# Optimization experiments

Measured on AMD Instinct MI355X. Metric: run time of the kernel, lower is better.

Reference implementation:

```python
import jax, jax.numpy as jnp
import numpy as np
from jax import lax

VOCAB, EMBED, HIDDEN, SEQ = 50257, 1024, 1024, 4096


def setup_inputs() -> dict:
    key = jax.random.key(0)
    ks = jax.random.split(key, 8)
    s = 0.02
    return {
        "input_seq": jax.random.randint(ks[0], (SEQ,), 0, VOCAB),
        "emb": jax.random.normal(ks[1], (VOCAB, EMBED), jnp.float32) * s,
        "Wrx": jax.random.normal(ks[2], (HIDDEN, EMBED), jnp.float32) * s,
        "Wrh": jax.random.normal(ks[3], (HIDDEN, HIDDEN), jnp.float32) * s,
        "Wzx": jax.random.normal(ks[4], (HIDDEN, EMBED), jnp.float32) * s,
        "Wzh": jax.random.normal(ks[5], (HIDDEN, HIDDEN), jnp.float32) * s,
        "Wx": jax.random.normal(ks[6], (HIDDEN, EMBED), jnp.float32) * s,
        "Wh": jax.random.normal(ks[7], (HIDDEN, HIDDEN), jnp.float32) * s,
    }


def reference(input_seq, emb, Wrx, Wrh, Wzx, Wzh, Wx, Wh):
    # Embed whole sequence at once: [S, E]
    x_seq = emb[input_seq]
    # Hoist input-side projections out of the recurrence (one GEMM each): [S, H]
    xr = x_seq @ Wrx.T
    xz = x_seq @ Wzx.T
    xh = x_seq @ Wx.T

    def step(h, xs):
        xr_t, xz_t, xh_t = xs
        z = jax.nn.sigmoid(xz_t + Wzh @ h)          # update gate
        r = jax.nn.sigmoid(xr_t + Wrh @ h)          # reset gate
        h_tilde = jnp.tanh(xh_t + Wh @ (r * h))     # candidate
        h_new = z * h + (1.0 - z) * h_tilde
        return h_new, None

    h0 = jnp.zeros((Wh.shape[0],), dtype=emb.dtype)
    h_final, _ = lax.scan(step, h0, (xr, xz, xh))
    return h_final
```

## Files before the change

kernel.cpp:

```cpp
#include <hip/hip_runtime.h>
#include <stdint.h>


#define HID    1024
#define SEQLEN 4096
#define NWG    128
#define RPW    8
#define BLOCK  256

typedef unsigned long long u64;

__global__ __launch_bounds__(BLOCK) void proj_gemm(
    const int* __restrict__ seq, const float* __restrict__ emb,
    const float* __restrict__ Wrx, const float* __restrict__ Wzx,
    const float* __restrict__ Wx,
    float* __restrict__ xr, float* __restrict__ xz, float* __restrict__ xh)
{
  __shared__ float As[32][68];
  __shared__ float Bs[32][68];
  __shared__ int   idx[64];

  const float* W = (blockIdx.z == 0) ? Wrx : (blockIdx.z == 1) ? Wzx : Wx;
  float*       C = (blockIdx.z == 0) ? xr  : (blockIdx.z == 1) ? xz  : xh;

  const int tid = threadIdx.x;
  const int t0 = blockIdx.y * 64;
  const int i0 = blockIdx.x * 64;
  if (tid < 64) idx[tid] = seq[t0 + tid];
  __syncthreads();

  float acc[4][4] = {};
  const int tx = tid & 15, ty = tid >> 4;
  const int c4 = (tid & 7) * 4;
  const int r8 = tid >> 3;

  for (int k0 = 0; k0 < HID; k0 += 32) {
    for (int l = 0; l < 2; ++l) {
      const int rr = r8 + l * 32;
      float4 av = *(const float4*)(emb + (size_t)idx[rr] * HID + k0 + c4);
      As[c4+0][rr]=av.x; As[c4+1][rr]=av.y; As[c4+2][rr]=av.z; As[c4+3][rr]=av.w;
      float4 bv = *(const float4*)(W + (size_t)(i0 + rr) * HID + k0 + c4);
      Bs[c4+0][rr]=bv.x; Bs[c4+1][rr]=bv.y; Bs[c4+2][rr]=bv.z; Bs[c4+3][rr]=bv.w;
    }
    __syncthreads();
    #pragma unroll
    for (int k = 0; k < 32; ++k) {
      float a[4], b[4];
      *(float4*)a = *(const float4*)&As[k][ty * 4];
      *(float4*)b = *(const float4*)&Bs[k][tx * 4];
      #pragma unroll
      for (int i = 0; i < 4; ++i)
        #pragma unroll
        for (int j = 0; j < 4; ++j)
          acc[i][j] = fmaf(a[i], b[j], acc[i][j]);
    }
    __syncthreads();
  }
  #pragma unroll
  for (int i = 0; i < 4; ++i) {
    float4 v = make_float4(acc[i][0], acc[i][1], acc[i][2], acc[i][3]);
    *(float4*)(C + (size_t)(t0 + ty * 4 + i) * HID + i0 + tx * 4) = v;
  }
}

__device__ __forceinline__ u64 pack_cell(float v, unsigned tag) {
  return ((u64)tag << 32) | (u64)__float_as_uint(v);
}

__device__ __forceinline__ void poll4(const u64* __restrict__ cells, int j0,
                                      unsigned want, float v[4], int* budget) {
  u64 c0 = 0, c1 = 0, c2 = 0, c3 = 0;
  bool d0 = false, d1 = false, d2 = false, d3 = false;
  for (;;) {
    if (!d0) { c0 = __hip_atomic_load(&cells[j0+0], __ATOMIC_RELAXED, __HIP_MEMORY_SCOPE_AGENT); d0 = (unsigned)(c0 >> 32) == want; }
    if (!d1) { c1 = __hip_atomic_load(&cells[j0+1], __ATOMIC_RELAXED, __HIP_MEMORY_SCOPE_AGENT); d1 = (unsigned)(c1 >> 32) == want; }
    if (!d2) { c2 = __hip_atomic_load(&cells[j0+2], __ATOMIC_RELAXED, __HIP_MEMORY_SCOPE_AGENT); d2 = (unsigned)(c2 >> 32) == want; }
    if (!d3) { c3 = __hip_atomic_load(&cells[j0+3], __ATOMIC_RELAXED, __HIP_MEMORY_SCOPE_AGENT); d3 = (unsigned)(c3 >> 32) == want; }
    if (d0 & d1 & d2 & d3) break;
    if (--(*budget) <= 0) break;
  }
  v[0] = __uint_as_float((unsigned)c0);
  v[1] = __uint_as_float((unsigned)c1);
  v[2] = __uint_as_float((unsigned)c2);
  v[3] = __uint_as_float((unsigned)c3);
}

__global__ __launch_bounds__(BLOCK) void rnn_scan(
    const float* __restrict__ Wzh, const float* __restrict__ Wrh,
    const float* __restrict__ Whh,
    const float* __restrict__ xz, const float* __restrict__ xr,
    const float* __restrict__ xh,
    u64* __restrict__ hcell,
    u64* __restrict__ rhcell,
    float* __restrict__ out)
{
  const int tid  = threadIdx.x;
  const int wave = tid >> 6, lane = tid & 63;
  const int g    = blockIdx.x;
  const int r0   = g * RPW;
  const int rowA = r0 + wave * 2;
  const int j0   = tid * 4;

  __shared__ float h_lds[HID];
  __shared__ float rh_lds[HID];

  float wgt[3][2][16];
  #pragma unroll
  for (int m = 0; m < 3; ++m) {
    const float* Wm = (m == 0) ? Wzh : (m == 1) ? Wrh : Whh;
    #pragma unroll
    for (int rr = 0; rr < 2; ++rr) {
      const float* p = Wm + (size_t)(rowA + rr) * HID + lane * 16;
      #pragma unroll
      for (int c = 0; c < 16; c += 4) {
        float4 v = *(const float4*)(p + c);
        wgt[m][rr][c+0] = v.x; wgt[m][rr][c+1] = v.y;
        wgt[m][rr][c+2] = v.z; wgt[m][rr][c+3] = v.w;
      }
    }
  }

  int budget = 1 << 22;
  float xzv[2], xrv[2], xhv[2], zv[2];

  for (int t = 1; t <= SEQLEN; ++t) {
    const u64* hsrc = hcell + ((t - 1) & 1) * HID;
    u64* rdst = rhcell + (t & 1) * HID;

    if (lane == 0) {
      #pragma unroll
      for (int rr = 0; rr < 2; ++rr) {
        xzv[rr] = xz[(size_t)(t - 1) * HID + rowA + rr];
        xrv[rr] = xr[(size_t)(t - 1) * HID + rowA + rr];
        xhv[rr] = xh[(size_t)(t - 1) * HID + rowA + rr];
      }
    }

    float hv[4];
    poll4(hsrc, j0, (unsigned)(t - 1), hv, &budget);
    *(float4*)&h_lds[j0] = make_float4(hv[0], hv[1], hv[2], hv[3]);
    __syncthreads();

    float hr[16];
    #pragma unroll
    for (int c = 0; c < 16; c += 4)
      *(float4*)&hr[c] = *(const float4*)&h_lds[lane * 16 + c];
    float az[2] = {0.f, 0.f}, ar[2] = {0.f, 0.f};
    #pragma unroll
    for (int rr = 0; rr < 2; ++rr)
      #pragma unroll
      for (int c = 0; c < 16; ++c) {
        az[rr] = fmaf(wgt[0][rr][c], hr[c], az[rr]);
        ar[rr] = fmaf(wgt[1][rr][c], hr[c], ar[rr]);
      }
    #pragma unroll
    for (int m = 1; m < 64; m <<= 1) {
      az[0] += __shfl_xor(az[0], m, 64);
      az[1] += __shfl_xor(az[1], m, 64);
      ar[0] += __shfl_xor(ar[0], m, 64);
      ar[1] += __shfl_xor(ar[1], m, 64);
    }
    if (lane == 0) {
      #pragma unroll
      for (int rr = 0; rr < 2; ++rr) {
        zv[rr]    = 1.f / (1.f + __expf(-(xzv[rr] + az[rr])));
        float rg  = 1.f / (1.f + __expf(-(xrv[rr] + ar[rr])));
        float rh  = rg * h_lds[rowA + rr];
        __hip_atomic_store(&rdst[rowA + rr], pack_cell(rh, (unsigned)t),
                           __ATOMIC_RELAXED, __HIP_MEMORY_SCOPE_AGENT);
      }
    }

    float rv[4];
    poll4(rdst, j0, (unsigned)t, rv, &budget);
    *(float4*)&rh_lds[j0] = make_float4(rv[0], rv[1], rv[2], rv[3]);
    __syncthreads();

    float rr16[16];
    #pragma unroll
    for (int c = 0; c < 16; c += 4)
      *(float4*)&rr16[c] = *(const float4*)&rh_lds[lane * 16 + c];
    float ac[2] = {0.f, 0.f};
    #pragma unroll
    for (int rr = 0; rr < 2; ++rr)
      #pragma unroll
      for (int c = 0; c < 16; ++c)
        ac[rr] = fmaf(wgt[2][rr][c], rr16[c], ac[rr]);
    #pragma unroll
    for (int m = 1; m < 64; m <<= 1) {
      ac[0] += __shfl_xor(ac[0], m, 64);
      ac[1] += __shfl_xor(ac[1], m, 64);
    }
    if (lane == 0) {
      #pragma unroll
      for (int rr = 0; rr < 2; ++rr) {
        float cand  = tanhf(xhv[rr] + ac[rr]);
        float hprev = h_lds[rowA + rr];
        float hn    = zv[rr] * hprev + (1.f - zv[rr]) * cand;
        __hip_atomic_store(&hcell[(t & 1) * HID + rowA + rr],
                           pack_cell(hn, (unsigned)t),
                           __ATOMIC_RELAXED, __HIP_MEMORY_SCOPE_AGENT);
        if (t == SEQLEN) out[rowA + rr] = hn;
      }
    }
    __syncthreads();
  }
}

extern "C" void kernel_launch(void* const* d_in, const int* in_sizes, int n_in,
                              void* d_out, int out_size, void* d_ws, size_t ws_size,
                              hipStream_t stream) {
  (void)in_sizes; (void)n_in; (void)out_size; (void)ws_size;

  const int*   seq = (const int*)d_in[0];
  const float* emb = (const float*)d_in[1];
  const float* Wrx = (const float*)d_in[2];
  const float* Wrh = (const float*)d_in[3];
  const float* Wzx = (const float*)d_in[4];
  const float* Wzh = (const float*)d_in[5];
  const float* Wx  = (const float*)d_in[6];
  const float* Wh  = (const float*)d_in[7];

  char* ws = (char*)d_ws;
  const size_t PROJ = (size_t)SEQLEN * HID * sizeof(float);
  float* xr = (float*)(ws);
  float* xz = (float*)(ws + PROJ);
  float* xh = (float*)(ws + 2 * PROJ);
  u64* hcell  = (u64*)(ws + 3 * PROJ);
  u64* rhcell = (u64*)(ws + 3 * PROJ + 2 * HID * sizeof(u64));

  hipMemsetAsync(hcell, 0xFF, 4 * HID * sizeof(u64), stream);
  hipMemsetAsync(hcell, 0x00, HID * sizeof(u64), stream);

  proj_gemm<<<dim3(HID / 64, SEQLEN / 64, 3), BLOCK, 0, stream>>>(
      seq, emb, Wrx, Wzx, Wx, xr, xz, xh);

  rnn_scan<<<dim3(NWG), BLOCK, 0, stream>>>(
      Wzh, Wrh, Wh, xz, xr, xh, hcell, rhcell, (float*)d_out);
}
```

Baseline: 26.33 ms.

## Replace tagged per-element cells with per-workgroup flags and coherent float buffers

Drops the 64-bit tagged value cells. Each workgroup now writes plain floats to double-buffered h and r*h arrays, then publishes one release flag per step. Consumers poll a single flag per pair of threads with s_sleep backoff and read the data with a cache-bypassing float4 load. This is meant to cut the number of polled atomic loads and halve the bytes moved per exchange, at the cost of an extra __syncthreads and a release-flag hop per phase. It also moves the weight and LDS indexing to a strided layout so LDS reads are bank-friendly.

```diff
diff --git a/kernel.cpp b/kernel.cpp
--- a/kernel.cpp
+++ b/kernel.cpp
@@ -63,35 +63,36 @@
   }
 }
 
-__device__ __forceinline__ u64 pack_cell(float v, unsigned tag) {
-  return ((u64)tag << 32) | (u64)__float_as_uint(v);
-}
-
-__device__ __forceinline__ void poll4(const u64* __restrict__ cells, int j0,
-                                      unsigned want, float v[4], int* budget) {
-  u64 c0 = 0, c1 = 0, c2 = 0, c3 = 0;
-  bool d0 = false, d1 = false, d2 = false, d3 = false;
+__device__ __forceinline__ float4 load_f4_coherent(const float* p) {
+  float4 v;
+  asm volatile("global_load_dwordx4 %0, %1, off sc0 sc1\n\ts_waitcnt vmcnt(0)"
+               : "=v"(v) : "v"(p) : "memory");
+  return v;
+}
+__device__ __forceinline__ void store_f2_coherent(float* p, float a, float b) {
+  u64 v = ((u64)__float_as_uint(b) << 32) | (u64)__float_as_uint(a);
+  __hip_atomic_store((u64*)p, v, __ATOMIC_RELAXED, __HIP_MEMORY_SCOPE_AGENT);
+}
+
+__device__ __forceinline__ void poll_flag(const u64* f, u64 want, int* budget) {
   for (;;) {
-    if (!d0) { c0 = __hip_atomic_load(&cells[j0+0], __ATOMIC_RELAXED, __HIP_MEMORY_SCOPE_AGENT); d0 = (unsigned)(c0 >> 32) == want; }
-    if (!d1) { c1 = __hip_atomic_load(&cells[j0+1], __ATOMIC_RELAXED, __HIP_MEMORY_SCOPE_AGENT); d1 = (unsigned)(c1 >> 32) == want; }
-    if (!d2) { c2 = __hip_atomic_load(&cells[j0+2], __ATOMIC_RELAXED, __HIP_MEMORY_SCOPE_AGENT); d2 = (unsigned)(c2 >> 32) == want; }
-    if (!d3) { c3 = __hip_atomic_load(&cells[j0+3], __ATOMIC_RELAXED, __HIP_MEMORY_SCOPE_AGENT); d3 = (unsigned)(c3 >> 32) == want; }
-    if (d0 & d1 & d2 & d3) break;
+    u64 v = __hip_atomic_load((u64*)f, __ATOMIC_RELAXED, __HIP_MEMORY_SCOPE_AGENT);
+    if (v >= want) break;
+    __builtin_amdgcn_s_sleep(1);
     if (--(*budget) <= 0) break;
   }
-  v[0] = __uint_as_float((unsigned)c0);
-  v[1] = __uint_as_float((unsigned)c1);
-  v[2] = __uint_as_float((unsigned)c2);
-  v[3] = __uint_as_float((unsigned)c3);
-}
-
-__global__ __launch_bounds__(BLOCK) void rnn_scan(
+  asm volatile("" ::: "memory");
+}
+
+__global__ __launch_bounds__(BLOCK, 1) void rnn_scan(
     const float* __restrict__ Wzh, const float* __restrict__ Wrh,
     const float* __restrict__ Whh,
     const float* __restrict__ xz, const float* __restrict__ xr,
     const float* __restrict__ xh,
-    u64* __restrict__ hcell,
-    u64* __restrict__ rhcell,
+    float* __restrict__ hbuf,
+    float* __restrict__ rhbuf,
+    u64* __restrict__ fh,
+    u64* __restrict__ frh,
     float* __restrict__ out)
 {
   const int tid  = threadIdx.x;
@@ -100,6 +101,7 @@
   const int r0   = g * RPW;
   const int rowA = r0 + wave * 2;
   const int j0   = tid * 4;
+  const int src  = tid >> 1;
 
   __shared__ float h_lds[HID];
   __shared__ float rh_lds[HID];
@@ -110,23 +112,20 @@
     const float* Wm = (m == 0) ? Wzh : (m == 1) ? Wrh : Whh;
     #pragma unroll
     for (int rr = 0; rr < 2; ++rr) {
-      const float* p = Wm + (size_t)(rowA + rr) * HID + lane * 16;
-      #pragma unroll
-      for (int c = 0; c < 16; c += 4) {
-        float4 v = *(const float4*)(p + c);
-        wgt[m][rr][c+0] = v.x; wgt[m][rr][c+1] = v.y;
-        wgt[m][rr][c+2] = v.z; wgt[m][rr][c+3] = v.w;
+      const float* p = Wm + (size_t)(rowA + rr) * HID + lane * 4;
+      #pragma unroll
+      for (int q = 0; q < 4; ++q) {
+        float4 v = *(const float4*)(p + q * 256);
+        wgt[m][rr][q*4+0] = v.x; wgt[m][rr][q*4+1] = v.y;
+        wgt[m][rr][q*4+2] = v.z; wgt[m][rr][q*4+3] = v.w;
       }
     }
   }
 
   int budget = 1 << 22;
-  float xzv[2], xrv[2], xhv[2], zv[2];
+  float xzv[2], xrv[2], xhv[2], zv[2], hprev[2];
 
   for (int t = 1; t <= SEQLEN; ++t) {
-    const u64* hsrc = hcell + ((t - 1) & 1) * HID;
-    u64* rdst = rhcell + (t & 1) * HID;
-
     if (lane == 0) {
       #pragma unroll
       for (int rr = 0; rr < 2; ++rr) {
@@ -136,15 +135,19 @@
       }
     }
 
-    float hv[4];
-    poll4(hsrc, j0, (unsigned)(t - 1), hv, &budget);
-    *(float4*)&h_lds[j0] = make_float4(hv[0], hv[1], hv[2], hv[3]);
+    if (t == 1) {
+      *(float4*)&h_lds[j0] = make_float4(0.f, 0.f, 0.f, 0.f);
+    } else {
+      poll_flag(&fh[src], (u64)(t - 1), &budget);
+      float4 hv = load_f4_coherent(hbuf + ((t - 1) & 1) * HID + j0);
+      *(float4*)&h_lds[j0] = hv;
+    }
     __syncthreads();
 
     float hr[16];
     #pragma unroll
-    for (int c = 0; c < 16; c += 4)
-      *(float4*)&hr[c] = *(const float4*)&h_lds[lane * 16 + c];
+    for (int q = 0; q < 4; ++q)
+      *(float4*)&hr[q*4] = *(const float4*)&h_lds[q * 256 + lane * 4];
     float az[2] = {0.f, 0.f}, ar[2] = {0.f, 0.f};
     #pragma unroll
     for (int rr = 0; rr < 2; ++rr)
@@ -161,25 +164,31 @@
       ar[1] += __shfl_xor(ar[1], m, 64);
     }
     if (lane == 0) {
+      float rh[2];
       #pragma unroll
       for (int rr = 0; rr < 2; ++rr) {
+        hprev[rr] = h_lds[rowA + rr];
         zv[rr]    = 1.f / (1.f + __expf(-(xzv[rr] + az[rr])));
         float rg  = 1.f / (1.f + __expf(-(xrv[rr] + ar[rr])));
-        float rh  = rg * h_lds[rowA + rr];
-        __hip_atomic_store(&rdst[rowA + rr], pack_cell(rh, (unsigned)t),
-                           __ATOMIC_RELAXED, __HIP_MEMORY_SCOPE_AGENT);
-      }
-    }
-
-    float rv[4];
-    poll4(rdst, j0, (unsigned)t, rv, &budget);
-    *(float4*)&rh_lds[j0] = make_float4(rv[0], rv[1], rv[2], rv[3]);
+        rh[rr]    = rg * hprev[rr];
+      }
+      store_f2_coherent(rhbuf + (t & 1) * HID + rowA, rh[0], rh[1]);
+    }
+    __syncthreads();
+    if (tid == 0)
+      __hip_atomic_store(&frh[g], (u64)t, __ATOMIC_RELEASE, __HIP_MEMORY_SCOPE_AGENT);
+
+    poll_flag(&frh[src], (u64)t, &budget);
+    {
+      float4 rv = load_f4_coherent(rhbuf + (t & 1) * HID + j0);
+      *(float4*)&rh_lds[j0] = rv;
+    }
     __syncthreads();
 
     float rr16[16];
     #pragma unroll
-    for (int c = 0; c < 16; c += 4)
-      *(float4*)&rr16[c] = *(const float4*)&rh_lds[lane * 16 + c];
+    for (int q = 0; q < 4; ++q)
+      *(float4*)&rr16[q*4] = *(const float4*)&rh_lds[q * 256 + lane * 4];
     float ac[2] = {0.f, 0.f};
     #pragma unroll
     for (int rr = 0; rr < 2; ++rr)
@@ -192,18 +201,18 @@
       ac[1] += __shfl_xor(ac[1], m, 64);
     }
     if (lane == 0) {
+      float hn[2];
       #pragma unroll
       for (int rr = 0; rr < 2; ++rr) {
-        float cand  = tanhf(xhv[rr] + ac[rr]);
-        float hprev = h_lds[rowA + rr];
-        float hn    = zv[rr] * hprev + (1.f - zv[rr]) * cand;
-        __hip_atomic_store(&hcell[(t & 1) * HID + rowA + rr],
-                           pack_cell(hn, (unsigned)t),
-                           __ATOMIC_RELAXED, __HIP_MEMORY_SCOPE_AGENT);
-        if (t == SEQLEN) out[rowA + rr] = hn;
-      }
-    }
-    __syncthreads();
+        float cand = tanhf(xhv[rr] + ac[rr]);
+        hn[rr]     = zv[rr] * hprev[rr] + (1.f - zv[rr]) * cand;
+      }
+      store_f2_coherent(hbuf + (t & 1) * HID + rowA, hn[0], hn[1]);
+      if (t == SEQLEN) { out[rowA] = hn[0]; out[rowA + 1] = hn[1]; }
+    }
+    __syncthreads();
+    if (tid == 0)
+      __hip_atomic_store(&fh[g], (u64)t, __ATOMIC_RELEASE, __HIP_MEMORY_SCOPE_AGENT);
   }
 }
 
@@ -223,18 +232,19 @@
 
   char* ws = (char*)d_ws;
   const size_t PROJ = (size_t)SEQLEN * HID * sizeof(float);
-  float* xr = (float*)(ws);
-  float* xz = (float*)(ws + PROJ);
-  float* xh = (float*)(ws + 2 * PROJ);
-  u64* hcell  = (u64*)(ws + 3 * PROJ);
-  u64* rhcell = (u64*)(ws + 3 * PROJ + 2 * HID * sizeof(u64));
-
-  hipMemsetAsync(hcell, 0xFF, 4 * HID * sizeof(u64), stream);
-  hipMemsetAsync(hcell, 0x00, HID * sizeof(u64), stream);
+  float* xr    = (float*)(ws);
+  float* xz    = (float*)(ws + PROJ);
+  float* xh    = (float*)(ws + 2 * PROJ);
+  float* hbuf  = (float*)(ws + 3 * PROJ);
+  float* rhbuf = (float*)(ws + 3 * PROJ + 2 * HID * sizeof(float));
+  u64*   fh    = (u64*)  (ws + 3 * PROJ + 4 * HID * sizeof(float));
+  u64*   frh   = fh + NWG;
+
+  (void)hipMemsetAsync(fh, 0, 2 * NWG * sizeof(u64), stream);
 
   proj_gemm<<<dim3(HID / 64, SEQLEN / 64, 3), BLOCK, 0, stream>>>(
       seq, emb, Wrx, Wzx, Wx, xr, xz, xh);
 
   rnn_scan<<<dim3(NWG), BLOCK, 0, stream>>>(
-      Wzh, Wrh, Wh, xz, xr, xh, hcell, rhcell, (float*)d_out);
-}
+      Wzh, Wrh, Wh, xz, xr, xh, hbuf, rhbuf, fh, frh, (float*)d_out);
+}
```

Result: slower. 36.20 ms (+37.5%).
